# Optimization experiments

Hardware: AMD Instinct MI355X
Metric: run time of the kernel (lower is better)

## Reference

```python
import jax, jax.numpy as jnp
import numpy as np

D_MODEL = 1024
NUM_HEADS = 16
D_K = D_MODEL // NUM_HEADS
ROPE_THETA = 10000.0


def apply_rope(x, pos):
    # x: [B, nh, S, d_k], pos: [S]
    d = x.shape[-1]
    inv_freq = ROPE_THETA ** (-jnp.arange(0, d, 2, dtype=jnp.float32) / d)  # [d/2]
    ang = pos.astype(jnp.float32)[:, None] * inv_freq[None, :]              # [S, d/2]
    cos, sin = jnp.cos(ang), jnp.sin(ang)
    x1, x2 = x[..., 0::2], x[..., 1::2]
    out_even = x1 * cos - x2 * sin
    out_odd = x1 * sin + x2 * cos
    return jnp.stack([out_even, out_odd], axis=-1).reshape(x.shape)


def setup_inputs() -> dict:
    key = jax.random.key(0)
    kx, kq, kk, kv, ko = jax.random.split(key, 5)
    B, S = 4, 2048
    std = np.sqrt(2.0 / (D_MODEL + D_MODEL))
    x = jax.random.normal(kx, (B, S, D_MODEL), dtype=jnp.float32)
    q_proj = jax.random.normal(kq, (D_MODEL, D_MODEL), dtype=jnp.float32) * std
    k_proj = jax.random.normal(kk, (D_MODEL, D_MODEL), dtype=jnp.float32) * std
    v_proj = jax.random.normal(kv, (D_MODEL, D_MODEL), dtype=jnp.float32) * std
    o_proj = jax.random.normal(ko, (D_MODEL, D_MODEL), dtype=jnp.float32) * std
    return {"x": x, "q_proj": q_proj, "k_proj": k_proj, "v_proj": v_proj, "o_proj": o_proj}


def reference(x, q_proj, k_proj, v_proj, o_proj):
    B, S, D = x.shape
    nh, dk = NUM_HEADS, D // NUM_HEADS
    # projections: weights stored [d_out, d_in] -> x @ W.T
    def split_heads(t):
        return t.reshape(B, S, nh, dk).transpose(0, 2, 1, 3)  # [B, nh, S, dk]
    q = split_heads(x @ q_proj.T)
    k = split_heads(x @ k_proj.T)
    v = split_heads(x @ v_proj.T)
    pos = jnp.arange(S)
    q = apply_rope(q, pos)
    k = apply_rope(k, pos)
    scores = jnp.einsum('bhqd,bhkd->bhqk', q, k) / jnp.sqrt(jnp.float32(dk))
    causal = jnp.tril(jnp.ones((S, S), dtype=bool))
    scores = jnp.where(causal, scores, -jnp.inf)
    attn = jax.nn.softmax(scores, axis=-1)
    out = jnp.einsum('bhqk,bhkd->bhqd', attn, v)          # [B, nh, S, dk]
    out = out.transpose(0, 2, 1, 3).reshape(B, S, D)      # merge heads
    return out @ o_proj.T
```

## Files before the change

kernel.cpp:

```cpp
#include <hip/hip_runtime.h>
#include <hip/hip_bf16.h>
#include <cstdint>


typedef __attribute__((ext_vector_type(8))) short short8;
typedef __attribute__((ext_vector_type(4))) float float4v;

#define MFMA16(a, b, c) __builtin_amdgcn_mfma_f32_16x16x32_bf16((a), (b), (c), 0, 0, 0)

__device__ __forceinline__ void glds16(const void* g, void* l) {
    __builtin_amdgcn_global_load_lds(
        (const __attribute__((address_space(1))) void*)g,
        (__attribute__((address_space(3))) void*)l, 16, 0, 0);
}

__device__ __forceinline__ unsigned int pk2(float a, float b) {
    __hip_bfloat162 h = __float22bfloat162_rn(make_float2(a, b));
    union { __hip_bfloat162 h; unsigned int u; } v; v.h = h;
    return v.u;
}

__device__ __forceinline__ unsigned short f2bf(float x) {
    union { float f; unsigned int u; } v; v.f = x;
    unsigned int r = (v.u + 0x7FFFu + ((v.u >> 16) & 1u)) >> 16;
    return (unsigned short)r;
}

__device__ __forceinline__ float bf2f(unsigned short b) {
    union { unsigned int u; float f; } v; v.u = ((unsigned int)b) << 16;
    return v.f;
}

__device__ __forceinline__ short8 load8f(const float* p) {
    const float4 f0 = *(const float4*)p;
    const float4 f1 = *(const float4*)(p + 4);
    union { short8 s; unsigned int u[4]; } r;
    r.u[0] = pk2(f0.x, f0.y);
    r.u[1] = pk2(f0.z, f0.w);
    r.u[2] = pk2(f1.x, f1.y);
    r.u[3] = pk2(f1.z, f1.w);
    return r.s;
}

__global__ __launch_bounds__(256) void convert_kernel(
    const float* __restrict__ in, __hip_bfloat16* __restrict__ out)
{
    const int idx = (blockIdx.x * 256 + threadIdx.x) * 8;
    *(short8*)(out + idx) = load8f(in + idx);
}

__global__ __launch_bounds__(256) void convert4_kernel(
    const float* __restrict__ a, const float* __restrict__ b,
    const float* __restrict__ c, const float* __restrict__ d,
    __hip_bfloat16* __restrict__ oa, __hip_bfloat16* __restrict__ ob,
    __hip_bfloat16* __restrict__ oc, __hip_bfloat16* __restrict__ od)
{
    const int m = blockIdx.x >> 9;
    const float* in = (m == 0) ? a : (m == 1) ? b : (m == 2) ? c : d;
    __hip_bfloat16* out = (m == 0) ? oa : (m == 1) ? ob : (m == 2) ? oc : od;
    const int idx = ((blockIdx.x & 511) * 256 + threadIdx.x) * 8;
    *(short8*)(out + idx) = load8f(in + idx);
}

__global__ __launch_bounds__(256) void rope_table_kernel(float2* __restrict__ table)
{
    const int idx = blockIdx.x * 256 + threadIdx.x;
    const int pos = idx >> 5, fi = idx & 31;
    const float f = exp2f(-(float)fi * (13.287712379549449f / 32.0f));
    float sn, cs;
    sincosf((float)pos * f, &sn, &cs);
    table[idx] = make_float2(cs, sn);
}

__global__ __launch_bounds__(256) void rope2_kernel(
    __hip_bfloat16* __restrict__ Qp, __hip_bfloat16* __restrict__ Kp,
    const float2* __restrict__ table)
{
    const int sel = blockIdx.x >> 14;
    __hip_bfloat16* T = sel ? Kp : Qp;
    const float scale = sel ? 1.0f : 0.18033688011112042f;
    const int idx = (blockIdx.x & 16383) * 256 + threadIdx.x;
    const int r = idx >> 9;
    const int p = idx & 511;
    const int h = p >> 5, i = p & 31;
    const float2 cs = table[(r & 2047) * 32 + i];
    unsigned short* ptr = (unsigned short*)T + (int64_t)r * 1024 + h * 64 + 2 * i;
    const ushort2 xv = *(const ushort2*)ptr;
    const float x1 = bf2f(xv.x), x2 = bf2f(xv.y);
    const unsigned int o = pk2((x1 * cs.x - x2 * cs.y) * scale,
                               (x1 * cs.y + x2 * cs.x) * scale);
    *(unsigned int*)ptr = o;
}

template<int BBF>
__global__ __launch_bounds__(256) void qkv_gemm(
    const __hip_bfloat16* __restrict__ Abf,
    const void* __restrict__ Wq, const void* __restrict__ Wk, const void* __restrict__ Wv,
    __hip_bfloat16* __restrict__ Qp, __hip_bfloat16* __restrict__ Kp,
    __hip_bfloat16* __restrict__ Vt)
{
    __shared__ unsigned short smem[12288];

    const int K = 1024;
    const int bm = blockIdx.x / 48, bn = blockIdx.x % 48;
    const int widx = bn >> 4;
    const int bcol0 = (bn & 15) * 64;
    const void* W = (widx == 0) ? Wq : (widx == 1) ? Wk : Wv;

    const int tid = threadIdx.x;
    const int wave = tid >> 6, lane = tid & 63;
    const int wm = (wave >> 1) * 64, wn = (wave & 1) * 32;
    const int m16 = lane & 15, quad = lane >> 4;

    const int grow = lane >> 3;
    const int gcolsw = ((lane & 7) ^ (lane >> 3)) * 8;
    const int srow = tid >> 3, scol = (tid & 7) * 8;

    float4v acc[4][2] = {};

    for (int k0 = 0; k0 < K; k0 += 64) {
        short8 rb[2];
        if (!BBF) {
            const float* Wf = (const float*)W;
#pragma unroll
            for (int t = 0; t < 2; t++)
                rb[t] = load8f(Wf + (int64_t)(bcol0 + t * 32 + srow) * K + k0 + scol);
        }
        __syncthreads();
        {
            const __hip_bfloat16* g = Abf + (int64_t)(bm * 128 + wave * 32 + grow) * K + k0 + gcolsw;
#pragma unroll
            for (int t = 0; t < 4; t++)
                glds16(g + (int64_t)(t * 8) * K, &smem[(wave * 32 + t * 8) * 64]);
        }
        if (BBF) {
            const __hip_bfloat16* g = (const __hip_bfloat16*)W +
                (int64_t)(bcol0 + wave * 16 + grow) * K + k0 + gcolsw;
#pragma unroll
            for (int t = 0; t < 2; t++)
                glds16(g + (int64_t)(t * 8) * K, &smem[8192 + (wave * 16 + t * 8) * 64]);
        } else {
#pragma unroll
            for (int t = 0; t < 2; t++) {
                const int r = t * 32 + srow;
                *(short8*)&smem[8192 + r * 64 + (scol ^ ((r & 7) * 8))] = rb[t];
            }
        }
        __syncthreads();

#pragma unroll
        for (int kk = 0; kk < 2; kk++) {
            const int ksw = (kk * 32 + quad * 8) ^ ((m16 & 7) * 8);
            short8 af[4], bf[2];
#pragma unroll
            for (int i = 0; i < 4; i++)
                af[i] = *(const short8*)&smem[(wm + i * 16 + m16) * 64 + ksw];
#pragma unroll
            for (int j = 0; j < 2; j++)
                bf[j] = *(const short8*)&smem[8192 + (wn + j * 16 + m16) * 64 + ksw];
#pragma unroll
            for (int i = 0; i < 4; i++)
#pragma unroll
                for (int j = 0; j < 2; j++)
                    acc[i][j] = MFMA16(af[i], bf[j], acc[i][j]);
        }
    }

    if (widx == 2) {
        __syncthreads();
#pragma unroll
        for (int i = 0; i < 4; i++)
#pragma unroll
            for (int j = 0; j < 2; j++) {
                const int col = wn + j * 16 + m16;
                const int key = (col & 7) * 8;
#pragma unroll
                for (int r = 0; r < 4; r++) {
                    const int row = wm + i * 16 + quad * 4 + r;
                    smem[col * 128 + (row ^ key)] = f2bf(acc[i][j][r]);
                }
            }
        __syncthreads();
        const int dc = tid >> 4;
        const int seg = (tid & 15) * 8;
#pragma unroll
        for (int pass = 0; pass < 4; pass++) {
            const int dcol = pass * 16 + dc;
            const short8 v = *(const short8*)&smem[dcol * 128 + (seg ^ ((dcol & 7) * 8))];
            *(short8*)((unsigned short*)Vt + (int64_t)(bcol0 + dcol) * 8192 + bm * 128 + seg) = v;
        }
    } else {
        __hip_bfloat16* dst = (widx == 0) ? Qp : Kp;
        const int row0 = bm * 128 + wm + quad * 4;
        const int col0 = bcol0 + wn + m16;
#pragma unroll
        for (int i = 0; i < 4; i++)
#pragma unroll
            for (int j = 0; j < 2; j++)
#pragma unroll
                for (int r = 0; r < 4; r++)
                    dst[(int64_t)(row0 + i * 16 + r) * 1024 + col0 + j * 16] =
                        __float2bfloat16(acc[i][j][r]);
    }
}

template<int BBF>
__global__ __launch_bounds__(256) void gemm_o(
    const __hip_bfloat16* __restrict__ Abf, const void* __restrict__ B,
    float* __restrict__ C, int M, int N, int K)
{
    __shared__ __hip_bfloat16 lA[128 * 64];
    __shared__ __hip_bfloat16 lB[64 * 64];

    const int nb = N >> 6;
    const int bm = blockIdx.x / nb, bn = blockIdx.x % nb;
    const int tid = threadIdx.x;
    const int wave = tid >> 6, lane = tid & 63;
    const int wm = (wave >> 1) * 64, wn = (wave & 1) * 32;
    const int m16 = lane & 15, quad = lane >> 4;
    const int grow = lane >> 3;
    const int gcolsw = ((lane & 7) ^ (lane >> 3)) * 8;
    const int srow = tid >> 3, scol = (tid & 7) * 8;

    float4v acc[4][2] = {};

    for (int k0 = 0; k0 < K; k0 += 64) {
        short8 rb[2];
        if (!BBF) {
            const float* Bf = (const float*)B;
#pragma unroll
            for (int t = 0; t < 2; t++)
                rb[t] = load8f(Bf + (int64_t)(bn * 64 + t * 32 + srow) * K + k0 + scol);
        }
        __syncthreads();
        {
            const __hip_bfloat16* g = Abf + (int64_t)(bm * 128 + wave * 32 + grow) * K + k0 + gcolsw;
#pragma unroll
            for (int t = 0; t < 4; t++)
                glds16(g + (int64_t)(t * 8) * K, &lA[(wave * 32 + t * 8) * 64]);
        }
        if (BBF) {
            const __hip_bfloat16* g = (const __hip_bfloat16*)B +
                (int64_t)(bn * 64 + wave * 16 + grow) * K + k0 + gcolsw;
#pragma unroll
            for (int t = 0; t < 2; t++)
                glds16(g + (int64_t)(t * 8) * K, &lB[(wave * 16 + t * 8) * 64]);
        } else {
#pragma unroll
            for (int t = 0; t < 2; t++) {
                const int r = t * 32 + srow;
                *(short8*)&lB[r * 64 + (scol ^ ((r & 7) * 8))] = rb[t];
            }
        }
        __syncthreads();

#pragma unroll
        for (int kk = 0; kk < 2; kk++) {
            const int ksw = (kk * 32 + quad * 8) ^ ((m16 & 7) * 8);
            short8 af[4], bf[2];
#pragma unroll
            for (int i = 0; i < 4; i++)
                af[i] = *(const short8*)&lA[(wm + i * 16 + m16) * 64 + ksw];
#pragma unroll
            for (int j = 0; j < 2; j++)
                bf[j] = *(const short8*)&lB[(wn + j * 16 + m16) * 64 + ksw];
#pragma unroll
            for (int i = 0; i < 4; i++)
#pragma unroll
                for (int j = 0; j < 2; j++)
                    acc[i][j] = MFMA16(af[i], bf[j], acc[i][j]);
        }
    }

    const int row0 = bm * 128 + wm + quad * 4;
    const int col0 = bn * 64 + wn + m16;
#pragma unroll
    for (int i = 0; i < 4; i++)
#pragma unroll
        for (int j = 0; j < 2; j++)
#pragma unroll
            for (int r = 0; r < 4; r++)
                C[(int64_t)(row0 + i * 16 + r) * N + col0 + j * 16] = acc[i][j][r];
}

__global__ __launch_bounds__(256) void attn_kernel(
    const __hip_bfloat16* __restrict__ Q,
    const __hip_bfloat16* __restrict__ Kg,
    const __hip_bfloat16* __restrict__ Vt,
    __hip_bfloat16* __restrict__ O,
    int S, int BS)
{
    const int g = blockIdx.x >> 6;
    const int qt = (g < 4) ? 15 - g : (g < 8) ? 11 - g : (g < 12) ? g : g - 12;
    const int bh = blockIdx.x & 63;
    const int b = bh >> 4, h = bh & 15;
    const int tid = threadIdx.x;
    const int wave = tid >> 6, lane = tid & 63;
    const int m16 = lane & 15, quad = lane >> 4;

    __shared__ __hip_bfloat16 lK[64 * 64];
    __shared__ __hip_bfloat16 lV[64 * 64];
    __shared__ __hip_bfloat16 lP[4][32 * 64];

    const int qrow0 = qt * 128 + wave * 32;
    const int64_t rowbase = (int64_t)b * S;

    short8 aq[2][2];
#pragma unroll
    for (int i = 0; i < 2; i++) {
        const __hip_bfloat16* qp = Q + (rowbase + qrow0 + i * 16 + m16) * 1024 + h * 64 + quad * 8;
        aq[i][0] = *(const short8*)qp;
        aq[i][1] = *(const short8*)(qp + 32);
    }

    float lsum[2] = {0.f, 0.f};
    float4v o_acc[2][4] = {};

    const int srow = tid >> 3;
    const int scol = (tid & 7) * 8;

    const int ktmax_blk = 2 * qt + 1;
    const int ktmax_w = 2 * qt + (wave >> 1);
    const int k8 = (m16 & 7) * 8;

    short8 pk0, pk1, pv0, pv1;
#define PREFETCH(KT)                                                                          \
    do {                                                                                      \
        pk0 = *(const short8*)(Kg + (rowbase + (KT) * 64 + srow) * 1024 + h * 64 + scol);     \
        pk1 = *(const short8*)(Kg + (rowbase + (KT) * 64 + srow + 32) * 1024 + h * 64 + scol);\
        pv0 = *(const short8*)(Vt + (int64_t)(h * 64 + srow) * BS + rowbase + (KT) * 64 + scol);      \
        pv1 = *(const short8*)(Vt + (int64_t)(h * 64 + srow + 32) * BS + rowbase + (KT) * 64 + scol); \
    } while (0)

    PREFETCH(0);

    for (int kt = 0; kt <= ktmax_blk; kt++) {
        __syncthreads();
        *(short8*)&lK[srow * 64 + (scol ^ ((srow & 7) * 8))] = pk0;
        *(short8*)&lK[(srow + 32) * 64 + (scol ^ (((srow + 32) & 7) * 8))] = pk1;
        *(short8*)&lV[srow * 64 + (scol ^ ((srow & 7) * 8))] = pv0;
        *(short8*)&lV[(srow + 32) * 64 + (scol ^ (((srow + 32) & 7) * 8))] = pv1;
        __syncthreads();

        if (kt < ktmax_blk) PREFETCH(kt + 1);

        if (kt <= ktmax_w) {
            float4v st[4][2] = {};
#pragma unroll
            for (int mi = 0; mi < 4; mi++) {
                const int n = mi * 16 + m16;
                const int sw = (n & 7) * 8;
                short8 k0 = *(const short8*)&lK[n * 64 + ((quad * 8) ^ sw)];
                short8 k1 = *(const short8*)&lK[n * 64 + ((32 + quad * 8) ^ sw)];
#pragma unroll
                for (int ni = 0; ni < 2; ni++) {
                    st[mi][ni] = MFMA16(k0, aq[ni][0], st[mi][ni]);
                    st[mi][ni] = MFMA16(k1, aq[ni][1], st[mi][ni]);
                }
            }

            const bool need_mask = (kt * 64 + 63 > qrow0);
#pragma unroll
            for (int ni = 0; ni < 2; ni++) {
                const int qg = qrow0 + ni * 16 + m16;
#pragma unroll
                for (int mi = 0; mi < 4; mi++) {
                    float p[4];
#pragma unroll
                    for (int r = 0; r < 4; r++) {
                        p[r] = __builtin_amdgcn_exp2f(st[mi][ni][r]);
                        if (need_mask) {
                            const int kvg = kt * 64 + mi * 16 + quad * 4 + r;
                            if (kvg > qg) p[r] = 0.0f;
                        }
                    }
                    lsum[ni] += (p[0] + p[1]) + (p[2] + p[3]);
                    uint2 w;
                    w.x = pk2(p[0], p[1]);
                    w.y = pk2(p[2], p[3]);
                    *(uint2*)&lP[wave][(ni * 16 + m16) * 64 + ((mi * 16 + quad * 4) ^ k8)] = w;
                }
            }

            short8 ap[2][2];
#pragma unroll
            for (int i = 0; i < 2; i++)
#pragma unroll
                for (int ks = 0; ks < 2; ks++)
                    ap[i][ks] = *(const short8*)
                        &lP[wave][(i * 16 + m16) * 64 + ((ks * 32 + quad * 8) ^ k8)];
#pragma unroll
            for (int jd = 0; jd < 4; jd++) {
                const int d = jd * 16 + m16;
                const int sw = (d & 7) * 8;
                short8 b0 = *(const short8*)&lV[d * 64 + ((quad * 8) ^ sw)];
                short8 b1 = *(const short8*)&lV[d * 64 + ((32 + quad * 8) ^ sw)];
#pragma unroll
                for (int i = 0; i < 2; i++) {
                    o_acc[i][jd] = MFMA16(ap[i][0], b0, o_acc[i][jd]);
                    o_acc[i][jd] = MFMA16(ap[i][1], b1, o_acc[i][jd]);
                }
            }
        }
    }
#undef PREFETCH

    float rinv[2];
#pragma unroll
    for (int ni = 0; ni < 2; ni++) {
        float v = lsum[ni];
        v += __shfl_xor(v, 16);
        v += __shfl_xor(v, 32);
        rinv[ni] = 1.0f / v;
    }
    float ri[2][4];
#pragma unroll
    for (int i = 0; i < 2; i++)
#pragma unroll
        for (int r = 0; r < 4; r++)
            ri[i][r] = __shfl(rinv[i], quad * 4 + r);

#pragma unroll
    for (int i = 0; i < 2; i++)
#pragma unroll
        for (int jd = 0; jd < 4; jd++)
#pragma unroll
            for (int r = 0; r < 4; r++) {
                const int row = qrow0 + i * 16 + quad * 4 + r;
                O[(rowbase + row) * 1024 + h * 64 + jd * 16 + m16] =
                    __float2bfloat16(o_acc[i][jd][r] * ri[i][r]);
            }
}

extern "C" void kernel_launch(void* const* d_in, const int* in_sizes, int n_in,
                              void* d_out, int out_size, void* d_ws, size_t ws_size,
                              hipStream_t stream)
{
    const float* x  = (const float*)d_in[0];
    const float* qw = (const float*)d_in[1];
    const float* kw = (const float*)d_in[2];
    const float* vw = (const float*)d_in[3];
    const float* ow = (const float*)d_in[4];

    const int BS = 8192, D = 1024, S = 2048;
    const size_t MiB = 1024 * 1024;

    char* ws = (char*)d_ws;
    __hip_bfloat16* xb  = (__hip_bfloat16*)(ws);
    __hip_bfloat16* Qb  = (__hip_bfloat16*)(ws + 16 * MiB);
    __hip_bfloat16* Kb  = (__hip_bfloat16*)(ws + 32 * MiB);
    __hip_bfloat16* Vtb = (__hip_bfloat16*)(ws + 48 * MiB);
    __hip_bfloat16* wqb = (__hip_bfloat16*)(ws + 64 * MiB);
    __hip_bfloat16* wkb = (__hip_bfloat16*)(ws + 66 * MiB);
    __hip_bfloat16* wvb = (__hip_bfloat16*)(ws + 68 * MiB);
    __hip_bfloat16* wob = (__hip_bfloat16*)(ws + 70 * MiB);
    float2* table = (float2*)(ws);
    const bool wbf = ws_size >= 72 * MiB;

    dim3 blk(256);
    convert_kernel<<<(BS * D) / 2048, blk, 0, stream>>>(x, xb);
    if (wbf) {
        convert4_kernel<<<4 * (D * D) / 2048, blk, 0, stream>>>(
            qw, kw, vw, ow, wqb, wkb, wvb, wob);
        qkv_gemm<1><<<64 * 48, blk, 0, stream>>>(xb, wqb, wkb, wvb, Qb, Kb, Vtb);
    } else {
        qkv_gemm<0><<<64 * 48, blk, 0, stream>>>(xb, qw, kw, vw, Qb, Kb, Vtb);
    }
    rope_table_kernel<<<256, blk, 0, stream>>>(table);
    rope2_kernel<<<2 * 16384, blk, 0, stream>>>(Qb, Kb, table);
    attn_kernel<<<4 * 16 * (S / 128), blk, 0, stream>>>(Qb, Kb, Vtb, Qb , S, BS);
    if (wbf) gemm_o<1><<<(BS / 128) * (D / 64), blk, 0, stream>>>(Qb, wob, (float*)d_out, BS, D, D);
    else     gemm_o<0><<<(BS / 128) * (D / 64), blk, 0, stream>>>(Qb, ow,  (float*)d_out, BS, D, D);
}
```

Before: 264.3 us.

## Fuse RoPE and Q scaling into QKV GEMM epilogue, merge table build into convert

Applies the RoPE rotation and softmax scale to Q/K directly in the QKV GEMM epilogue. Each lane gets its even/odd partner value via a lane shuffle and reads cos/sin from a precomputed table. This removes the separate rope2 kernel, which read and rewrote all of Q and K in bf16. The rope table build is folded into the x-conversion launch, dropping another launch. The table now lives in scratch space inside the output buffer, which gemm_o later overwrites. The epilogue gains a table load and a shuffle per element.

```diff
diff --git a/kernel.cpp b/kernel.cpp
--- a/kernel.cpp
+++ b/kernel.cpp
@@ -42,11 +42,21 @@
     return r.s;
 }
 
-__global__ __launch_bounds__(256) void convert_kernel(
-    const float* __restrict__ in, __hip_bfloat16* __restrict__ out)
-{
-    const int idx = (blockIdx.x * 256 + threadIdx.x) * 8;
-    *(short8*)(out + idx) = load8f(in + idx);
+__global__ __launch_bounds__(256) void convert_x_table(
+    const float* __restrict__ in, __hip_bfloat16* __restrict__ out,
+    float2* __restrict__ table)
+{
+    if (blockIdx.x < 4096) {
+        const int idx = (blockIdx.x * 256 + threadIdx.x) * 8;
+        *(short8*)(out + idx) = load8f(in + idx);
+    } else {
+        const int idx = (blockIdx.x - 4096) * 256 + threadIdx.x;
+        const int pos = idx >> 5, fi = idx & 31;
+        const float f = exp2f(-(float)fi * (13.287712379549449f / 32.0f));
+        float sn, cs;
+        sincosf((float)pos * f, &sn, &cs);
+        table[idx] = make_float2(cs, sn);
+    }
 }
 
 __global__ __launch_bounds__(256) void convert4_kernel(
@@ -62,42 +72,12 @@
     *(short8*)(out + idx) = load8f(in + idx);
 }
 
-__global__ __launch_bounds__(256) void rope_table_kernel(float2* __restrict__ table)
-{
-    const int idx = blockIdx.x * 256 + threadIdx.x;
-    const int pos = idx >> 5, fi = idx & 31;
-    const float f = exp2f(-(float)fi * (13.287712379549449f / 32.0f));
-    float sn, cs;
-    sincosf((float)pos * f, &sn, &cs);
-    table[idx] = make_float2(cs, sn);
-}
-
-__global__ __launch_bounds__(256) void rope2_kernel(
-    __hip_bfloat16* __restrict__ Qp, __hip_bfloat16* __restrict__ Kp,
-    const float2* __restrict__ table)
-{
-    const int sel = blockIdx.x >> 14;
-    __hip_bfloat16* T = sel ? Kp : Qp;
-    const float scale = sel ? 1.0f : 0.18033688011112042f;
-    const int idx = (blockIdx.x & 16383) * 256 + threadIdx.x;
-    const int r = idx >> 9;
-    const int p = idx & 511;
-    const int h = p >> 5, i = p & 31;
-    const float2 cs = table[(r & 2047) * 32 + i];
-    unsigned short* ptr = (unsigned short*)T + (int64_t)r * 1024 + h * 64 + 2 * i;
-    const ushort2 xv = *(const ushort2*)ptr;
-    const float x1 = bf2f(xv.x), x2 = bf2f(xv.y);
-    const unsigned int o = pk2((x1 * cs.x - x2 * cs.y) * scale,
-                               (x1 * cs.y + x2 * cs.x) * scale);
-    *(unsigned int*)ptr = o;
-}
-
 template<int BBF>
 __global__ __launch_bounds__(256) void qkv_gemm(
     const __hip_bfloat16* __restrict__ Abf,
     const void* __restrict__ Wq, const void* __restrict__ Wk, const void* __restrict__ Wv,
     __hip_bfloat16* __restrict__ Qp, __hip_bfloat16* __restrict__ Kp,
-    __hip_bfloat16* __restrict__ Vt)
+    __hip_bfloat16* __restrict__ Vt, const float2* __restrict__ table)
 {
     __shared__ unsigned short smem[12288];
 
@@ -191,16 +171,25 @@
         }
     } else {
         __hip_bfloat16* dst = (widx == 0) ? Qp : Kp;
+        const float scale = (widx == 0) ? 0.18033688011112042f : 1.0f;
+        const float sgn = (m16 & 1) ? 1.0f : -1.0f;
         const int row0 = bm * 128 + wm + quad * 4;
         const int col0 = bcol0 + wn + m16;
 #pragma unroll
         for (int i = 0; i < 4; i++)
 #pragma unroll
-            for (int j = 0; j < 2; j++)
-#pragma unroll
-                for (int r = 0; r < 4; r++)
-                    dst[(int64_t)(row0 + i * 16 + r) * 1024 + col0 + j * 16] =
-                        __float2bfloat16(acc[i][j][r]);
+            for (int j = 0; j < 2; j++) {
+                const int ifq = ((wn + j * 16 + m16) & 63) >> 1;
+#pragma unroll
+                for (int r = 0; r < 4; r++) {
+                    const float v = acc[i][j][r] * scale;
+                    const float vp = __shfl_xor(v, 1);
+                    const int row = row0 + i * 16 + r;
+                    const float2 cs = table[(row & 2047) * 32 + ifq];
+                    const float out = v * cs.x + sgn * vp * cs.y;
+                    dst[(int64_t)row * 1024 + col0 + j * 16] = __float2bfloat16(out);
+                }
+            }
     }
 }
 
@@ -454,20 +443,18 @@
     __hip_bfloat16* wkb = (__hip_bfloat16*)(ws + 66 * MiB);
     __hip_bfloat16* wvb = (__hip_bfloat16*)(ws + 68 * MiB);
     __hip_bfloat16* wob = (__hip_bfloat16*)(ws + 70 * MiB);
-    float2* table = (float2*)(ws);
+    float2* table = (float2*)((char*)d_out + 31 * MiB);
     const bool wbf = ws_size >= 72 * MiB;
 
     dim3 blk(256);
-    convert_kernel<<<(BS * D) / 2048, blk, 0, stream>>>(x, xb);
+    convert_x_table<<<4096 + 256, blk, 0, stream>>>(x, xb, table);
     if (wbf) {
         convert4_kernel<<<4 * (D * D) / 2048, blk, 0, stream>>>(
             qw, kw, vw, ow, wqb, wkb, wvb, wob);
-        qkv_gemm<1><<<64 * 48, blk, 0, stream>>>(xb, wqb, wkb, wvb, Qb, Kb, Vtb);
+        qkv_gemm<1><<<64 * 48, blk, 0, stream>>>(xb, wqb, wkb, wvb, Qb, Kb, Vtb, table);
     } else {
-        qkv_gemm<0><<<64 * 48, blk, 0, stream>>>(xb, qw, kw, vw, Qb, Kb, Vtb);
-    }
-    rope_table_kernel<<<256, blk, 0, stream>>>(table);
-    rope2_kernel<<<2 * 16384, blk, 0, stream>>>(Qb, Kb, table);
+        qkv_gemm<0><<<64 * 48, blk, 0, stream>>>(xb, qw, kw, vw, Qb, Kb, Vtb, table);
+    }
     attn_kernel<<<4 * 16 * (S / 128), blk, 0, stream>>>(Qb, Kb, Vtb, Qb , S, BS);
     if (wbf) gemm_o<1><<<(BS / 128) * (D / 64), blk, 0, stream>>>(Qb, wob, (float*)d_out, BS, D, D);
     else     gemm_o<0><<<(BS / 128) * (D / 64), blk, 0, stream>>>(Qb, ow,  (float*)d_out, BS, D, D);
```

Result: faster. 250.6 us (median of 2 runs) (-5.2%).
